# Kernel tuning notes

Hardware: AMD Instinct MI355X
Metric: run time of the kernel (lower is better)

## Reference

```python
import jax, jax.numpy as jnp
import numpy as np

N_NODES = 50000


def gcn_conv(x, src, dst, W, b, n_nodes):
    """PyG-style GCNConv: x' = D^-1/2 (A + I) D^-1/2 (x W) + b.
    src/dst already include self-loops."""
    h = x @ W  # [N, C_out]
    # symmetric normalization from degree (with self-loops, unit edge weight)
    deg = jax.ops.segment_sum(jnp.ones_like(dst, dtype=h.dtype), dst,
                              num_segments=n_nodes)  # [N]
    dinv = jnp.where(deg > 0, jax.lax.rsqrt(deg), 0.0)
    norm = dinv[src] * dinv[dst]  # [E]
    msg = h[src] * norm[:, None]  # gather + scale, [E, C_out]
    out = jax.ops.segment_sum(msg, dst, num_segments=n_nodes)  # scatter-add
    return out + b


def setup_inputs() -> dict:
    key = jax.random.key(0)
    k1, k2, k3, k4, k5, k6 = jax.random.split(key, 6)
    in_c, hid_c, out_c = 128, 64, 64
    x = jax.random.normal(k1, (N_NODES, in_c), dtype=jnp.float32)
    edge_index = jax.random.randint(k2, (2, 800000), 0, N_NODES, dtype=jnp.int64)
    # Glorot-ish init for weights, zeros for bias (as PyG default)
    W1 = jax.random.normal(k3, (in_c, hid_c), dtype=jnp.float32) / np.sqrt(in_c)
    b1 = jnp.zeros((hid_c,), dtype=jnp.float32)
    W2 = jax.random.normal(k4, (hid_c, out_c), dtype=jnp.float32) / np.sqrt(hid_c)
    b2 = jnp.zeros((out_c,), dtype=jnp.float32)
    return {"x": x, "edge_index": edge_index, "W1": W1, "b1": b1,
            "W2": W2, "b2": b2}


def reference(x, edge_index, W1, b1, W2, b2):
    n = x.shape[0]
    loops = jnp.arange(n, dtype=edge_index.dtype)
    src = jnp.concatenate([edge_index[0], loops])  # add self-loops
    dst = jnp.concatenate([edge_index[1], loops])
    h = gcn_conv(x, src, dst, W1, b1, n)
    h = jax.nn.relu(h)
    return gcn_conv(h, src, dst, W2, b2, n)
```

## Files before the change

### kernel.cpp

```cpp
#include <hip/hip_runtime.h>
#include <hip/hip_fp16.h>


#define C_HID 64

static inline size_t alignup(size_t x) { return (x + 255) & ~(size_t)255; }

typedef __attribute__((address_space(3))) unsigned int lds_uint;
typedef __attribute__((address_space(1))) const unsigned int glob_uint;

__device__ __forceinline__ int blockScanIncl256(int v, int* wsum) {
    const int lane = threadIdx.x & 63, wav = threadIdx.x >> 6;
    int s = v;
#pragma unroll
    for (int off = 1; off < 64; off <<= 1) {
        int t = __shfl_up(s, off);
        if (lane >= off) s += t;
    }
    if (lane == 63) wsum[wav] = s;
    __syncthreads();
    if (wav == 0 && lane < 4) {
        int ws = wsum[lane];
#pragma unroll
        for (int off = 1; off < 4; off <<= 1) {
            int t = __shfl_up(ws, off);
            if (lane >= off) ws += t;
        }
        wsum[lane] = ws;
    }
    __syncthreads();
    return (wav ? wsum[wav - 1] : 0) + s;
}

template <int K>
__global__ __launch_bounds__(256) void gemm1_hist_kernel(
    const float* __restrict__ X, const float* __restrict__ W,
    const int* __restrict__ dst, __half* __restrict__ outh,
    int* __restrict__ S, int n, int E, int ePer, int nb) {
    constexpr int KP = K + 4;
    __shared__ float Xs[64 * KP];
    __shared__ float Ws[K * 64];
    __shared__ int h[256];
    const int t = threadIdx.x;
    const int lane = t & 63;
    const int wav = t >> 6;

    if ((int)blockIdx.x < nb) {
        h[t] = 0;
        __syncthreads();
        int beg = blockIdx.x * ePer, end = min(E, beg + ePer);
        for (int e = beg + t; e < end; e += 256)
            atomicAdd(&h[dst[e] >> 8], 1);
        __syncthreads();
        for (int b = t; b < nb; b += 256)
            S[(size_t)b * nb + blockIdx.x] = h[b];
        return;
    }

    const int row0 = ((int)blockIdx.x - nb) * 64;
    {
        const char* gb = (const char*)W;
        char* lb = (char*)Ws;
        for (int off = wav * 1024; off < K * 64 * 4; off += 4096)
            __builtin_amdgcn_global_load_lds((glob_uint*)(gb + off + lane * 16),
                                             (lds_uint*)(lb + off), 16, 0, 0);
    }
    if (row0 + 64 <= n) {
        const float4* g4 = (const float4*)(X + (size_t)row0 * K);
        for (int i = t; i < 64 * (K / 4); i += 256) {
            float4 v = g4[i];
            int r = i / (K / 4), k0 = (i % (K / 4)) * 4;
            *(float4*)&Xs[r * KP + k0] = v;
        }
    } else {
        for (int i = t; i < 64 * K; i += 256) {
            int r = i / K, k = i % K;
            Xs[r * KP + k] = (row0 + r < n) ? X[(size_t)(row0 + r) * K + k] : 0.0f;
        }
    }
    __syncthreads();

    const int tx = t & 15;
    const int ty = t >> 4;
    float acc[4][4] = {{0.f}};
#pragma unroll 2
    for (int k0 = 0; k0 < K; k0 += 4) {
        float4 a0 = *(const float4*)&Xs[(4 * ty + 0) * KP + k0];
        float4 a1 = *(const float4*)&Xs[(4 * ty + 1) * KP + k0];
        float4 a2 = *(const float4*)&Xs[(4 * ty + 2) * KP + k0];
        float4 a3 = *(const float4*)&Xs[(4 * ty + 3) * KP + k0];
        float4 b0 = *(const float4*)&Ws[(k0 + 0) * 64 + 4 * tx];
        float4 b1 = *(const float4*)&Ws[(k0 + 1) * 64 + 4 * tx];
        float4 b2 = *(const float4*)&Ws[(k0 + 2) * 64 + 4 * tx];
        float4 b3 = *(const float4*)&Ws[(k0 + 3) * 64 + 4 * tx];
        const float* ap[4] = {(const float*)&a0, (const float*)&a1,
                              (const float*)&a2, (const float*)&a3};
        const float* bp[4] = {(const float*)&b0, (const float*)&b1,
                              (const float*)&b2, (const float*)&b3};
#pragma unroll
        for (int r = 0; r < 4; ++r)
#pragma unroll
            for (int kk = 0; kk < 4; ++kk) {
                float av = ap[r][kk];
#pragma unroll
                for (int c = 0; c < 4; ++c)
                    acc[r][c] = fmaf(av, bp[kk][c], acc[r][c]);
            }
    }
#pragma unroll
    for (int r = 0; r < 4; ++r) {
        int row = row0 + 4 * ty + r;
        if (row < n) {
            __half2 p01 = __floats2half2_rn(acc[r][0], acc[r][1]);
            __half2 p23 = __floats2half2_rn(acc[r][2], acc[r][3]);
            float2 st;
            ((__half2*)&st)[0] = p01;
            ((__half2*)&st)[1] = p23;
            *(float2*)&outh[(size_t)row * 64 + 4 * tx] = st;
        }
    }
}

__global__ __launch_bounds__(256) void scan_rows_kernel(
    int* __restrict__ S, int* __restrict__ T, int nb) {
    __shared__ int wsum[4];
    const int b = blockIdx.x, t = threadIdx.x;
    int v = (t < nb) ? S[(size_t)b * nb + t] : 0;
    int incl = blockScanIncl256(v, wsum);
    if (t < nb) S[(size_t)b * nb + t] = incl - v;
    if (t == 0) T[b] = wsum[3];
}

__global__ __launch_bounds__(256) void scatter_kernel(
    const int* __restrict__ src, const int* __restrict__ dst, int E, int ePer,
    const int* __restrict__ S, const int* __restrict__ T,
    unsigned* __restrict__ ebuf, int nb) {
    __shared__ int arr[256];
    __shared__ int wsum[4];
    const int b = blockIdx.x, t = threadIdx.x;
    int tv = (t < nb) ? T[t] : 0;
    int tincl = blockScanIncl256(tv, wsum);
    int texcl = tincl - tv;
    if (t < nb) arr[t] = S[(size_t)t * nb + b] + texcl;
    __syncthreads();
    int beg = b * ePer, end = min(E, beg + ePer);
    for (int e = beg + t; e < end; e += 256) {
        int d = dst[e];
        int s = src[e];
        int pos = atomicAdd(&arr[d >> 8], 1);
        ebuf[pos] = ((unsigned)s << 8) | (unsigned)(d & 255);
    }
}

__global__ __launch_bounds__(256) void build_kernel(
    const unsigned* __restrict__ ebuf, const int* __restrict__ T,
    int* __restrict__ row_ptr, float* __restrict__ dinv,
    int* __restrict__ esrc, int n, int nb) {
    __shared__ int arr[256];
    __shared__ int texcl_s[256];
    __shared__ int wsum[4];
    const int b = blockIdx.x, t = threadIdx.x;
    const int node0 = b << 8;

    int tv = (t < nb) ? T[t] : 0;
    int tincl = blockScanIncl256(tv, wsum);
    texcl_s[t] = tincl - tv;
    __syncthreads();
    const int ebeg = texcl_s[b];
    const int eend = (b + 1 < nb) ? texcl_s[b + 1] : wsum[3];

    arr[t] = 0;
    __syncthreads();
    for (int e = ebeg + t; e < eend; e += 256)
        atomicAdd(&arr[ebuf[e] & 255], 1);
    __syncthreads();
    int deg = arr[t];
    int incl = blockScanIncl256(deg, wsum);
    int excl = incl - deg;
    __syncthreads();
    arr[t] = ebeg + excl;
    int v = node0 + t;
    if (v < n) {
        row_ptr[v + 1] = ebeg + incl;
        dinv[v] = rsqrtf(1.0f + (float)deg);
        if (v == 0) row_ptr[0] = 0;
    }
    __syncthreads();
    for (int e = ebeg + t; e < eend; e += 256) {
        unsigned p = ebuf[e];
        int pos = atomicAdd(&arr[p & 255], 1);
        esrc[pos] = (int)(p >> 8);
    }
}

__global__ __launch_bounds__(256) void agg1_gemm2_kernel(
    const __half* __restrict__ g1, const int* __restrict__ row_ptr,
    const int* __restrict__ esrc, const float* __restrict__ dinv,
    const float* __restrict__ b1, const float* __restrict__ W2,
    __half* __restrict__ g2, int n) {
    __shared__ float Bt[64][68];
    __shared__ float Ws2[64 * 64];
    const int t = threadIdx.x, lane = t & 63, wav = t >> 6;

    {
        const char* gb = (const char*)W2;
        char* lb = (char*)Ws2;
        for (int off = wav * 1024; off < 64 * 64 * 4; off += 4096)
            __builtin_amdgcn_global_load_lds((glob_uint*)(gb + off + lane * 16),
                                             (lds_uint*)(lb + off), 16, 0, 0);
    }

    const int g = t >> 2;
    const int c = t & 3;
    const int row0 = blockIdx.x * 64;
    const int v = row0 + g;
    const float4* __restrict__ hs4 = (const float4*)g1;

    if (v < n) {
        float acc[16];
        float dv0 = dinv[v];
        {
            size_t rb = (size_t)v * 8 + 2 * c;
            float4 r0 = hs4[rb], r1 = hs4[rb + 1];
            const __half2* h0 = (const __half2*)&r0;
            const __half2* h1 = (const __half2*)&r1;
#pragma unroll
            for (int q = 0; q < 4; ++q) {
                float2 f0 = __half22float2(h0[q]);
                float2 f1 = __half22float2(h1[q]);
                acc[2 * q] = f0.x * dv0;     acc[2 * q + 1] = f0.y * dv0;
                acc[8 + 2 * q] = f1.x * dv0; acc[9 + 2 * q] = f1.y * dv0;
            }
        }
        const int beg = row_ptr[v], end = row_ptr[v + 1];
        int j = beg;
        for (; j + 4 <= end; j += 4) {
            int s0 = esrc[j], s1 = esrc[j + 1], s2 = esrc[j + 2], s3 = esrc[j + 3];
            float d0 = dinv[s0], d1 = dinv[s1], d2 = dinv[s2], d3 = dinv[s3];
            size_t rb0 = (size_t)s0 * 8 + 2 * c, rb1 = (size_t)s1 * 8 + 2 * c;
            size_t rb2 = (size_t)s2 * 8 + 2 * c, rb3 = (size_t)s3 * 8 + 2 * c;
            float4 a0 = hs4[rb0], a1 = hs4[rb0 + 1];
            float4 b0 = hs4[rb1], b1v = hs4[rb1 + 1];
            float4 c0 = hs4[rb2], c1 = hs4[rb2 + 1];
            float4 e0 = hs4[rb3], e1 = hs4[rb3 + 1];
            const __half2 *pa0 = (const __half2*)&a0, *pa1 = (const __half2*)&a1;
            const __half2 *pb0 = (const __half2*)&b0, *pb1 = (const __half2*)&b1v;
            const __half2 *pc0 = (const __half2*)&c0, *pc1 = (const __half2*)&c1;
            const __half2 *pe0 = (const __half2*)&e0, *pe1 = (const __half2*)&e1;
#pragma unroll
            for (int q = 0; q < 4; ++q) {
                float2 f;
                f = __half22float2(pa0[q]);
                acc[2 * q] = fmaf(f.x, d0, acc[2 * q]);
                acc[2 * q + 1] = fmaf(f.y, d0, acc[2 * q + 1]);
                f = __half22float2(pa1[q]);
                acc[8 + 2 * q] = fmaf(f.x, d0, acc[8 + 2 * q]);
                acc[9 + 2 * q] = fmaf(f.y, d0, acc[9 + 2 * q]);
                f = __half22float2(pb0[q]);
                acc[2 * q] = fmaf(f.x, d1, acc[2 * q]);
                acc[2 * q + 1] = fmaf(f.y, d1, acc[2 * q + 1]);
                f = __half22float2(pb1[q]);
                acc[8 + 2 * q] = fmaf(f.x, d1, acc[8 + 2 * q]);
                acc[9 + 2 * q] = fmaf(f.y, d1, acc[9 + 2 * q]);
                f = __half22float2(pc0[q]);
                acc[2 * q] = fmaf(f.x, d2, acc[2 * q]);
                acc[2 * q + 1] = fmaf(f.y, d2, acc[2 * q + 1]);
                f = __half22float2(pc1[q]);
                acc[8 + 2 * q] = fmaf(f.x, d2, acc[8 + 2 * q]);
                acc[9 + 2 * q] = fmaf(f.y, d2, acc[9 + 2 * q]);
                f = __half22float2(pe0[q]);
                acc[2 * q] = fmaf(f.x, d3, acc[2 * q]);
                acc[2 * q + 1] = fmaf(f.y, d3, acc[2 * q + 1]);
                f = __half22float2(pe1[q]);
                acc[8 + 2 * q] = fmaf(f.x, d3, acc[8 + 2 * q]);
                acc[9 + 2 * q] = fmaf(f.y, d3, acc[9 + 2 * q]);
            }
        }
        for (; j < end; ++j) {
            int s0 = esrc[j];
            float d0 = dinv[s0];
            size_t rb0 = (size_t)s0 * 8 + 2 * c;
            float4 a0 = hs4[rb0], a1 = hs4[rb0 + 1];
            const __half2 *pa0 = (const __half2*)&a0, *pa1 = (const __half2*)&a1;
#pragma unroll
            for (int q = 0; q < 4; ++q) {
                float2 f;
                f = __half22float2(pa0[q]);
                acc[2 * q] = fmaf(f.x, d0, acc[2 * q]);
                acc[2 * q + 1] = fmaf(f.y, d0, acc[2 * q + 1]);
                f = __half22float2(pa1[q]);
                acc[8 + 2 * q] = fmaf(f.x, d0, acc[8 + 2 * q]);
                acc[9 + 2 * q] = fmaf(f.y, d0, acc[9 + 2 * q]);
            }
        }
        const float* bb = b1 + c * 16;
#pragma unroll
        for (int u = 0; u < 4; ++u) {
            float4 w;
            w.x = fmaxf(fmaf(acc[4 * u + 0], dv0, bb[4 * u + 0]), 0.f);
            w.y = fmaxf(fmaf(acc[4 * u + 1], dv0, bb[4 * u + 1]), 0.f);
            w.z = fmaxf(fmaf(acc[4 * u + 2], dv0, bb[4 * u + 2]), 0.f);
            w.w = fmaxf(fmaf(acc[4 * u + 3], dv0, bb[4 * u + 3]), 0.f);
            *(float4*)&Bt[g][c * 16 + 4 * u] = w;
        }
    } else {
#pragma unroll
        for (int u = 0; u < 4; ++u)
            *(float4*)&Bt[g][c * 16 + 4 * u] = make_float4(0.f, 0.f, 0.f, 0.f);
    }
    __syncthreads();

    const int tx = t & 15;
    const int ty = t >> 4;
    float a2[4][4] = {{0.f}};
#pragma unroll 2
    for (int k0 = 0; k0 < 64; k0 += 4) {
        float4 x0 = *(const float4*)&Bt[4 * ty + 0][k0];
        float4 x1 = *(const float4*)&Bt[4 * ty + 1][k0];
        float4 x2 = *(const float4*)&Bt[4 * ty + 2][k0];
        float4 x3 = *(const float4*)&Bt[4 * ty + 3][k0];
        float4 w0 = *(const float4*)&Ws2[(k0 + 0) * 64 + 4 * tx];
        float4 w1 = *(const float4*)&Ws2[(k0 + 1) * 64 + 4 * tx];
        float4 w2 = *(const float4*)&Ws2[(k0 + 2) * 64 + 4 * tx];
        float4 w3 = *(const float4*)&Ws2[(k0 + 3) * 64 + 4 * tx];
        const float* xp[4] = {(const float*)&x0, (const float*)&x1,
                              (const float*)&x2, (const float*)&x3};
        const float* wp[4] = {(const float*)&w0, (const float*)&w1,
                              (const float*)&w2, (const float*)&w3};
#pragma unroll
        for (int r = 0; r < 4; ++r)
#pragma unroll
            for (int kk = 0; kk < 4; ++kk) {
                float av = xp[r][kk];
#pragma unroll
                for (int cc = 0; cc < 4; ++cc)
                    a2[r][cc] = fmaf(av, wp[kk][cc], a2[r][cc]);
            }
    }
#pragma unroll
    for (int r = 0; r < 4; ++r) {
        int row = row0 + 4 * ty + r;
        if (row < n) {
            float dv = dinv[row];
            __half2 p01 = __floats2half2_rn(a2[r][0] * dv, a2[r][1] * dv);
            __half2 p23 = __floats2half2_rn(a2[r][2] * dv, a2[r][3] * dv);
            float2 st;
            ((__half2*)&st)[0] = p01;
            ((__half2*)&st)[1] = p23;
            *(float2*)&g2[(size_t)row * 64 + 4 * tx] = st;
        }
    }
}

__global__ __launch_bounds__(256) void aggregate2_kernel(
    const __half* __restrict__ hs,
    const int* __restrict__ row_ptr,
    const int* __restrict__ esrc,
    const float* __restrict__ dinv,
    const float* __restrict__ bias,
    float* __restrict__ out, int n) {
    const int v = blockIdx.x * 32 + (threadIdx.x >> 3);
    if (v >= n) return;
    const int c8 = threadIdx.x & 7;
    const float4* __restrict__ hs4 = (const float4*)hs;

    const int beg = row_ptr[v];
    const int end = row_ptr[v + 1];

    float acc[8];
    {
        float4 raw = hs4[(size_t)v * 8 + c8];
        const __half2* hp = (const __half2*)&raw;
#pragma unroll
        for (int q = 0; q < 4; ++q) {
            float2 f = __half22float2(hp[q]);
            acc[2 * q] = f.x; acc[2 * q + 1] = f.y;
        }
    }

    int j = beg;
    for (; j + 4 <= end; j += 4) {
        int s0 = esrc[j], s1 = esrc[j + 1], s2 = esrc[j + 2], s3 = esrc[j + 3];
        float4 r0 = hs4[(size_t)s0 * 8 + c8];
        float4 r1 = hs4[(size_t)s1 * 8 + c8];
        float4 r2 = hs4[(size_t)s2 * 8 + c8];
        float4 r3 = hs4[(size_t)s3 * 8 + c8];
        const __half2* h0 = (const __half2*)&r0;
        const __half2* h1 = (const __half2*)&r1;
        const __half2* h2 = (const __half2*)&r2;
        const __half2* h3 = (const __half2*)&r3;
#pragma unroll
        for (int q = 0; q < 4; ++q) {
            float2 f0 = __half22float2(h0[q]);
            float2 f1 = __half22float2(h1[q]);
            float2 f2 = __half22float2(h2[q]);
            float2 f3 = __half22float2(h3[q]);
            acc[2 * q]     += (f0.x + f1.x) + (f2.x + f3.x);
            acc[2 * q + 1] += (f0.y + f1.y) + (f2.y + f3.y);
        }
    }
    for (; j < end; ++j) {
        int s0 = esrc[j];
        float4 r0 = hs4[(size_t)s0 * 8 + c8];
        const __half2* h0 = (const __half2*)&r0;
#pragma unroll
        for (int q = 0; q < 4; ++q) {
            float2 f0 = __half22float2(h0[q]);
            acc[2 * q] += f0.x;
            acc[2 * q + 1] += f0.y;
        }
    }

    float dv = dinv[v];
    float4 b0 = *(const float4*)(bias + c8 * 8);
    float4 b1v = *(const float4*)(bias + c8 * 8 + 4);
    float4 o0, o1;
    o0.x = fmaf(acc[0], dv, b0.x); o0.y = fmaf(acc[1], dv, b0.y);
    o0.z = fmaf(acc[2], dv, b0.z); o0.w = fmaf(acc[3], dv, b0.w);
    o1.x = fmaf(acc[4], dv, b1v.x); o1.y = fmaf(acc[5], dv, b1v.y);
    o1.z = fmaf(acc[6], dv, b1v.z); o1.w = fmaf(acc[7], dv, b1v.w);
    float4* op = (float4*)(out + (size_t)v * 64 + c8 * 8);
    op[0] = o0;
    op[1] = o1;
}

extern "C" void kernel_launch(void* const* d_in, const int* in_sizes, int n_in,
                              void* d_out, int out_size, void* d_ws, size_t ws_size,
                              hipStream_t stream) {
    const float* x  = (const float*)d_in[0];
    const int*   ei = (const int*)d_in[1];
    const float* W1 = (const float*)d_in[2];
    const float* b1 = (const float*)d_in[3];
    const float* W2 = (const float*)d_in[4];
    const float* b2 = (const float*)d_in[5];
    float* out = (float*)d_out;

    const int C_IN = 128;
    const int n = in_sizes[0] / C_IN;
    const int E = in_sizes[1] / 2;
    const int* src = ei;
    const int* dst = ei + E;

    const int nb = (n + 255) >> 8;
    const int ngb = (n + 63) / 64;
    const int ePer = (E + nb - 1) / nb;

    char* w = (char*)d_ws;
    float*    dinv    = (float*)w;    w += alignup((size_t)n * sizeof(float));
    __half*   g1      = (__half*)w;   w += alignup((size_t)n * C_HID * sizeof(__half));
    __half*   g2      = (__half*)w;   w += alignup((size_t)n * C_HID * sizeof(__half));
    int*      row_ptr = (int*)w;      w += alignup((size_t)(n + 1) * sizeof(int));
    int*      S       = (int*)w;      w += alignup((size_t)nb * nb * sizeof(int));
    int*      T       = (int*)w;      w += alignup((size_t)(nb + 1) * sizeof(int));
    unsigned* ebuf    = (unsigned*)w; w += alignup((size_t)E * sizeof(unsigned));
    int*      esrc    = (int*)w;

    gemm1_hist_kernel<128><<<nb + ngb, 256, 0, stream>>>(
        x, W1, dst, g1, S, n, E, ePer, nb);

    scan_rows_kernel<<<nb, 256, 0, stream>>>(S, T, nb);
    scatter_kernel<<<nb, 256, 0, stream>>>(src, dst, E, ePer, S, T, ebuf, nb);
    build_kernel<<<nb, 256, 0, stream>>>(ebuf, T, row_ptr, dinv, esrc, n, nb);

    agg1_gemm2_kernel<<<ngb, 256, 0, stream>>>(
        g1, row_ptr, esrc, dinv, b1, W2, g2, n);

    aggregate2_kernel<<<(n + 31) / 32, 256, 0, stream>>>(
        g2, row_ptr, esrc, dinv, b2, out, n);
}
```

Baseline: 161.4 us.

## Refine CSR bucketing to 64-node bins, prescale g1 by dinv, stage edges in LDS

The counting-sort CSR build now uses 64-node buckets with a fixed 512 edge chunks instead of 256-node buckets tied to the bucket count. This gives more parallel blocks in the build kernel and smaller per-block histograms. The build kernel now pre-scales g1 rows by dinv, so the first aggregation no longer gathers dinv per edge. Both aggregation kernels stage their block's edge-source list in shared memory when it fits, with a fallback to global reads. The cost is larger shared arrays, extra scan work over up to 1024 buckets, and an extra read-modify-write pass over g1.

```diff
diff --git a/kernel.cpp b/kernel.cpp
--- a/kernel.cpp
+++ b/kernel.cpp
@@ -3,6 +3,9 @@
 
 
 #define C_HID 64
+#define NCHUNK 512
+#define ES3 1280
+#define ES4 768
 
 static inline size_t alignup(size_t x) { return (x + 255) & ~(size_t)255; }
 
@@ -40,24 +43,24 @@
     constexpr int KP = K + 4;
     __shared__ float Xs[64 * KP];
     __shared__ float Ws[K * 64];
-    __shared__ int h[256];
+    __shared__ int h[1024];
     const int t = threadIdx.x;
     const int lane = t & 63;
     const int wav = t >> 6;
 
-    if ((int)blockIdx.x < nb) {
-        h[t] = 0;
+    if ((int)blockIdx.x < NCHUNK) {
+        for (int i = t; i < nb; i += 256) h[i] = 0;
         __syncthreads();
         int beg = blockIdx.x * ePer, end = min(E, beg + ePer);
         for (int e = beg + t; e < end; e += 256)
-            atomicAdd(&h[dst[e] >> 8], 1);
+            atomicAdd(&h[dst[e] >> 6], 1);
         __syncthreads();
         for (int b = t; b < nb; b += 256)
-            S[(size_t)b * nb + blockIdx.x] = h[b];
+            S[(size_t)b * NCHUNK + blockIdx.x] = h[b];
         return;
     }
 
-    const int row0 = ((int)blockIdx.x - nb) * 64;
+    const int row0 = ((int)blockIdx.x - NCHUNK) * 64;
     {
         const char* gb = (const char*)W;
         char* lb = (char*)Ws;
@@ -122,12 +125,19 @@
 }
 
 __global__ __launch_bounds__(256) void scan_rows_kernel(
-    int* __restrict__ S, int* __restrict__ T, int nb) {
+    int* __restrict__ S, int* __restrict__ T) {
     __shared__ int wsum[4];
     const int b = blockIdx.x, t = threadIdx.x;
-    int v = (t < nb) ? S[(size_t)b * nb + t] : 0;
-    int incl = blockScanIncl256(v, wsum);
-    if (t < nb) S[(size_t)b * nb + t] = incl - v;
+    int4 v = make_int4(0, 0, 0, 0);
+    if (t < NCHUNK / 4) v = ((const int4*)(S + (size_t)b * NCHUNK))[t];
+    int p1 = v.x + v.y, p2 = p1 + v.z, p3 = p2 + v.w;
+    int incl = blockScanIncl256(p3, wsum);
+    int excl = incl - p3;
+    if (t < NCHUNK / 4) {
+        int4 o;
+        o.x = excl; o.y = excl + v.x; o.z = excl + p1; o.w = excl + p2;
+        ((int4*)(S + (size_t)b * NCHUNK))[t] = o;
+    }
     if (t == 0) T[b] = wsum[3];
 }
 
@@ -135,61 +145,160 @@
     const int* __restrict__ src, const int* __restrict__ dst, int E, int ePer,
     const int* __restrict__ S, const int* __restrict__ T,
     unsigned* __restrict__ ebuf, int nb) {
-    __shared__ int arr[256];
+    __shared__ int tmp[1024];
+    __shared__ int arr[1024];
     __shared__ int wsum[4];
     const int b = blockIdx.x, t = threadIdx.x;
-    int tv = (t < nb) ? T[t] : 0;
-    int tincl = blockScanIncl256(tv, wsum);
-    int texcl = tincl - tv;
-    if (t < nb) arr[t] = S[(size_t)t * nb + b] + texcl;
+    {
+        int a0 = (4 * t + 0 < nb) ? T[4 * t + 0] : 0;
+        int a1 = (4 * t + 1 < nb) ? T[4 * t + 1] : 0;
+        int a2 = (4 * t + 2 < nb) ? T[4 * t + 2] : 0;
+        int a3 = (4 * t + 3 < nb) ? T[4 * t + 3] : 0;
+        int p1 = a0 + a1, p2 = p1 + a2, p3 = p2 + a3;
+        int incl = blockScanIncl256(p3, wsum);
+        int excl = incl - p3;
+        tmp[4 * t + 0] = excl;
+        tmp[4 * t + 1] = excl + a0;
+        tmp[4 * t + 2] = excl + p1;
+        tmp[4 * t + 3] = excl + p2;
+    }
+    __syncthreads();
+    for (int i = t; i < nb; i += 256)
+        arr[i] = S[(size_t)i * NCHUNK + b] + tmp[i];
     __syncthreads();
     int beg = b * ePer, end = min(E, beg + ePer);
     for (int e = beg + t; e < end; e += 256) {
         int d = dst[e];
         int s = src[e];
-        int pos = atomicAdd(&arr[d >> 8], 1);
-        ebuf[pos] = ((unsigned)s << 8) | (unsigned)(d & 255);
+        int pos = atomicAdd(&arr[d >> 6], 1);
+        ebuf[pos] = ((unsigned)s << 6) | (unsigned)(d & 63);
     }
 }
 
 __global__ __launch_bounds__(256) void build_kernel(
     const unsigned* __restrict__ ebuf, const int* __restrict__ T,
     int* __restrict__ row_ptr, float* __restrict__ dinv,
-    int* __restrict__ esrc, int n, int nb) {
-    __shared__ int arr[256];
-    __shared__ int texcl_s[256];
+    int* __restrict__ esrc, __half* __restrict__ g1, int n, int nb) {
+    __shared__ int tmp[1024];
+    __shared__ int cnt[64];
+    __shared__ int cur[64];
+    __shared__ float dvs[64];
     __shared__ int wsum[4];
     const int b = blockIdx.x, t = threadIdx.x;
-    const int node0 = b << 8;
-
-    int tv = (t < nb) ? T[t] : 0;
-    int tincl = blockScanIncl256(tv, wsum);
-    texcl_s[t] = tincl - tv;
-    __syncthreads();
-    const int ebeg = texcl_s[b];
-    const int eend = (b + 1 < nb) ? texcl_s[b + 1] : wsum[3];
-
-    arr[t] = 0;
-    __syncthreads();
+    {
+        int a0 = (4 * t + 0 < nb) ? T[4 * t + 0] : 0;
+        int a1 = (4 * t + 1 < nb) ? T[4 * t + 1] : 0;
+        int a2 = (4 * t + 2 < nb) ? T[4 * t + 2] : 0;
+        int a3 = (4 * t + 3 < nb) ? T[4 * t + 3] : 0;
+        int p1 = a0 + a1, p2 = p1 + a2, p3 = p2 + a3;
+        int incl = blockScanIncl256(p3, wsum);
+        int excl = incl - p3;
+        tmp[4 * t + 0] = excl + a0;
+        tmp[4 * t + 1] = excl + p1;
+        tmp[4 * t + 2] = excl + p2;
+        tmp[4 * t + 3] = excl + p3;
+    }
+    if (t < 64) cnt[t] = 0;
+    __syncthreads();
+    const int ebeg = b ? tmp[b - 1] : 0;
+    const int eend = tmp[b];
+
     for (int e = ebeg + t; e < eend; e += 256)
-        atomicAdd(&arr[ebuf[e] & 255], 1);
-    __syncthreads();
-    int deg = arr[t];
-    int incl = blockScanIncl256(deg, wsum);
-    int excl = incl - deg;
-    __syncthreads();
-    arr[t] = ebeg + excl;
-    int v = node0 + t;
-    if (v < n) {
-        row_ptr[v + 1] = ebeg + incl;
-        dinv[v] = rsqrtf(1.0f + (float)deg);
-        if (v == 0) row_ptr[0] = 0;
+        atomicAdd(&cnt[ebuf[e] & 63], 1);
+    __syncthreads();
+    if (t < 64) {
+        int deg = cnt[t];
+        int s = deg;
+#pragma unroll
+        for (int off = 1; off < 64; off <<= 1) {
+            int x = __shfl_up(s, off);
+            if (t >= off) s += x;
+        }
+        cur[t] = ebeg + s - deg;
+        float dv = rsqrtf(1.0f + (float)deg);
+        dvs[t] = dv;
+        int v = (b << 6) + t;
+        if (v < n) {
+            row_ptr[v + 1] = ebeg + s;
+            dinv[v] = dv;
+            if (v == 0) row_ptr[0] = 0;
+        }
     }
     __syncthreads();
     for (int e = ebeg + t; e < eend; e += 256) {
         unsigned p = ebuf[e];
-        int pos = atomicAdd(&arr[p & 255], 1);
-        esrc[pos] = (int)(p >> 8);
+        int pos = atomicAdd(&cur[p & 63], 1);
+        esrc[pos] = (int)(p >> 6);
+    }
+    {
+        const int row = t >> 2, q = t & 3;
+        const int v = (b << 6) + row;
+        if (v < n) {
+            float dv = dvs[row];
+            float4* gp = (float4*)(g1 + (size_t)v * 64 + q * 16);
+            float4 r0 = gp[0], r1 = gp[1];
+            __half2* h0 = (__half2*)&r0;
+            __half2* h1 = (__half2*)&r1;
+#pragma unroll
+            for (int i2 = 0; i2 < 4; ++i2) {
+                float2 f0 = __half22float2(h0[i2]);
+                float2 f1 = __half22float2(h1[i2]);
+                h0[i2] = __floats2half2_rn(f0.x * dv, f0.y * dv);
+                h1[i2] = __floats2half2_rn(f1.x * dv, f1.y * dv);
+            }
+            gp[0] = r0;
+            gp[1] = r1;
+        }
+    }
+}
+
+template <bool LDSE>
+__device__ __forceinline__ void agg1_body(
+    const float4* __restrict__ hs4, const int* es, const int* __restrict__ esg,
+    int beg0, int beg, int end, int c, float acc[16]) {
+    int j = beg;
+    for (; j + 4 <= end; j += 4) {
+        int s0, s1, s2, s3;
+        if (LDSE) {
+            s0 = es[j]; s1 = es[j + 1]; s2 = es[j + 2]; s3 = es[j + 3];
+        } else {
+            s0 = esg[beg0 + j]; s1 = esg[beg0 + j + 1];
+            s2 = esg[beg0 + j + 2]; s3 = esg[beg0 + j + 3];
+        }
+        size_t rb0 = (size_t)s0 * 8 + 2 * c, rb1 = (size_t)s1 * 8 + 2 * c;
+        size_t rb2 = (size_t)s2 * 8 + 2 * c, rb3 = (size_t)s3 * 8 + 2 * c;
+        float4 a0 = hs4[rb0], a1 = hs4[rb0 + 1];
+        float4 b0 = hs4[rb1], b1v = hs4[rb1 + 1];
+        float4 c0 = hs4[rb2], c1 = hs4[rb2 + 1];
+        float4 e0 = hs4[rb3], e1 = hs4[rb3 + 1];
+        const __half2 *pa0 = (const __half2*)&a0, *pa1 = (const __half2*)&a1;
+        const __half2 *pb0 = (const __half2*)&b0, *pb1 = (const __half2*)&b1v;
+        const __half2 *pc0 = (const __half2*)&c0, *pc1 = (const __half2*)&c1;
+        const __half2 *pe0 = (const __half2*)&e0, *pe1 = (const __half2*)&e1;
+#pragma unroll
+        for (int q = 0; q < 4; ++q) {
+            float2 f;
+            f = __half22float2(pa0[q]); acc[2 * q] += f.x; acc[2 * q + 1] += f.y;
+            f = __half22float2(pa1[q]); acc[8 + 2 * q] += f.x; acc[9 + 2 * q] += f.y;
+            f = __half22float2(pb0[q]); acc[2 * q] += f.x; acc[2 * q + 1] += f.y;
+            f = __half22float2(pb1[q]); acc[8 + 2 * q] += f.x; acc[9 + 2 * q] += f.y;
+            f = __half22float2(pc0[q]); acc[2 * q] += f.x; acc[2 * q + 1] += f.y;
+            f = __half22float2(pc1[q]); acc[8 + 2 * q] += f.x; acc[9 + 2 * q] += f.y;
+            f = __half22float2(pe0[q]); acc[2 * q] += f.x; acc[2 * q + 1] += f.y;
+            f = __half22float2(pe1[q]); acc[8 + 2 * q] += f.x; acc[9 + 2 * q] += f.y;
+        }
+    }
+    for (; j < end; ++j) {
+        int s0 = LDSE ? es[j] : esg[beg0 + j];
+        size_t rb0 = (size_t)s0 * 8 + 2 * c;
+        float4 a0 = hs4[rb0], a1 = hs4[rb0 + 1];
+        const __half2 *pa0 = (const __half2*)&a0, *pa1 = (const __half2*)&a1;
+#pragma unroll
+        for (int q = 0; q < 4; ++q) {
+            float2 f;
+            f = __half22float2(pa0[q]); acc[2 * q] += f.x; acc[2 * q + 1] += f.y;
+            f = __half22float2(pa1[q]); acc[8 + 2 * q] += f.x; acc[9 + 2 * q] += f.y;
+        }
     }
 }
 
@@ -200,7 +309,17 @@
     __half* __restrict__ g2, int n) {
     __shared__ float Bt[64][68];
     __shared__ float Ws2[64 * 64];
+    __shared__ int es[ES3];
     const int t = threadIdx.x, lane = t & 63, wav = t >> 6;
+    const int row0 = blockIdx.x * 64;
+
+    const int beg0 = row_ptr[row0];
+    const int end0 = row_ptr[min(row0 + 64, n)];
+    const int tot = end0 - beg0;
+    const bool uselds = (tot <= ES3);
+    if (uselds)
+        for (int i = t; i < tot; i += 256) es[i] = esrc[beg0 + i];
+    __syncthreads();
 
     {
         const char* gb = (const char*)W2;
@@ -212,13 +331,11 @@
 
     const int g = t >> 2;
     const int c = t & 3;
-    const int row0 = blockIdx.x * 64;
     const int v = row0 + g;
     const float4* __restrict__ hs4 = (const float4*)g1;
 
     if (v < n) {
         float acc[16];
-        float dv0 = dinv[v];
         {
             size_t rb = (size_t)v * 8 + 2 * c;
             float4 r0 = hs4[rb], r1 = hs4[rb + 1];
@@ -228,71 +345,15 @@
             for (int q = 0; q < 4; ++q) {
                 float2 f0 = __half22float2(h0[q]);
                 float2 f1 = __half22float2(h1[q]);
-                acc[2 * q] = f0.x * dv0;     acc[2 * q + 1] = f0.y * dv0;
-                acc[8 + 2 * q] = f1.x * dv0; acc[9 + 2 * q] = f1.y * dv0;
+                acc[2 * q] = f0.x;     acc[2 * q + 1] = f0.y;
+                acc[8 + 2 * q] = f1.x; acc[9 + 2 * q] = f1.y;
             }
         }
-        const int beg = row_ptr[v], end = row_ptr[v + 1];
-        int j = beg;
-        for (; j + 4 <= end; j += 4) {
-            int s0 = esrc[j], s1 = esrc[j + 1], s2 = esrc[j + 2], s3 = esrc[j + 3];
-            float d0 = dinv[s0], d1 = dinv[s1], d2 = dinv[s2], d3 = dinv[s3];
-            size_t rb0 = (size_t)s0 * 8 + 2 * c, rb1 = (size_t)s1 * 8 + 2 * c;
-            size_t rb2 = (size_t)s2 * 8 + 2 * c, rb3 = (size_t)s3 * 8 + 2 * c;
-            float4 a0 = hs4[rb0], a1 = hs4[rb0 + 1];
-            float4 b0 = hs4[rb1], b1v = hs4[rb1 + 1];
-            float4 c0 = hs4[rb2], c1 = hs4[rb2 + 1];
-            float4 e0 = hs4[rb3], e1 = hs4[rb3 + 1];
-            const __half2 *pa0 = (const __half2*)&a0, *pa1 = (const __half2*)&a1;
-            const __half2 *pb0 = (const __half2*)&b0, *pb1 = (const __half2*)&b1v;
-            const __half2 *pc0 = (const __half2*)&c0, *pc1 = (const __half2*)&c1;
-            const __half2 *pe0 = (const __half2*)&e0, *pe1 = (const __half2*)&e1;
-#pragma unroll
-            for (int q = 0; q < 4; ++q) {
-                float2 f;
-                f = __half22float2(pa0[q]);
-                acc[2 * q] = fmaf(f.x, d0, acc[2 * q]);
-                acc[2 * q + 1] = fmaf(f.y, d0, acc[2 * q + 1]);
-                f = __half22float2(pa1[q]);
-                acc[8 + 2 * q] = fmaf(f.x, d0, acc[8 + 2 * q]);
-                acc[9 + 2 * q] = fmaf(f.y, d0, acc[9 + 2 * q]);
-                f = __half22float2(pb0[q]);
-                acc[2 * q] = fmaf(f.x, d1, acc[2 * q]);
-                acc[2 * q + 1] = fmaf(f.y, d1, acc[2 * q + 1]);
-                f = __half22float2(pb1[q]);
-                acc[8 + 2 * q] = fmaf(f.x, d1, acc[8 + 2 * q]);
-                acc[9 + 2 * q] = fmaf(f.y, d1, acc[9 + 2 * q]);
-                f = __half22float2(pc0[q]);
-                acc[2 * q] = fmaf(f.x, d2, acc[2 * q]);
-                acc[2 * q + 1] = fmaf(f.y, d2, acc[2 * q + 1]);
-                f = __half22float2(pc1[q]);
-                acc[8 + 2 * q] = fmaf(f.x, d2, acc[8 + 2 * q]);
-                acc[9 + 2 * q] = fmaf(f.y, d2, acc[9 + 2 * q]);
-                f = __half22float2(pe0[q]);
-                acc[2 * q] = fmaf(f.x, d3, acc[2 * q]);
-                acc[2 * q + 1] = fmaf(f.y, d3, acc[2 * q + 1]);
-                f = __half22float2(pe1[q]);
-                acc[8 + 2 * q] = fmaf(f.x, d3, acc[8 + 2 * q]);
-                acc[9 + 2 * q] = fmaf(f.y, d3, acc[9 + 2 * q]);
-            }
-        }
-        for (; j < end; ++j) {
-            int s0 = esrc[j];
-            float d0 = dinv[s0];
-            size_t rb0 = (size_t)s0 * 8 + 2 * c;
-            float4 a0 = hs4[rb0], a1 = hs4[rb0 + 1];
-            const __half2 *pa0 = (const __half2*)&a0, *pa1 = (const __half2*)&a1;
-#pragma unroll
-            for (int q = 0; q < 4; ++q) {
-                float2 f;
-                f = __half22float2(pa0[q]);
-                acc[2 * q] = fmaf(f.x, d0, acc[2 * q]);
-                acc[2 * q + 1] = fmaf(f.y, d0, acc[2 * q + 1]);
-                f = __half22float2(pa1[q]);
-                acc[8 + 2 * q] = fmaf(f.x, d0, acc[8 + 2 * q]);
-                acc[9 + 2 * q] = fmaf(f.y, d0, acc[9 + 2 * q]);
-            }
-        }
+        const int beg = row_ptr[v] - beg0;
+        const int end = row_ptr[v + 1] - beg0;
+        if (uselds) agg1_body<true>(hs4, es, esrc, beg0, beg, end, c, acc);
+        else        agg1_body<false>(hs4, es, esrc, beg0, beg, end, c, acc);
+        const float dv0 = dinv[v];
         const float* bb = b1 + c * 16;
 #pragma unroll
         for (int u = 0; u < 4; ++u) {
@@ -352,35 +413,19 @@
     }
 }
 
-__global__ __launch_bounds__(256) void aggregate2_kernel(
-    const __half* __restrict__ hs,
-    const int* __restrict__ row_ptr,
-    const int* __restrict__ esrc,
-    const float* __restrict__ dinv,
-    const float* __restrict__ bias,
-    float* __restrict__ out, int n) {
-    const int v = blockIdx.x * 32 + (threadIdx.x >> 3);
-    if (v >= n) return;
-    const int c8 = threadIdx.x & 7;
-    const float4* __restrict__ hs4 = (const float4*)hs;
-
-    const int beg = row_ptr[v];
-    const int end = row_ptr[v + 1];
-
-    float acc[8];
-    {
-        float4 raw = hs4[(size_t)v * 8 + c8];
-        const __half2* hp = (const __half2*)&raw;
-#pragma unroll
-        for (int q = 0; q < 4; ++q) {
-            float2 f = __half22float2(hp[q]);
-            acc[2 * q] = f.x; acc[2 * q + 1] = f.y;
-        }
-    }
-
+template <bool LDSE>
+__device__ __forceinline__ void agg2_body(
+    const float4* __restrict__ hs4, const int* es, const int* __restrict__ esg,
+    int beg0, int beg, int end, int c8, float acc[8]) {
     int j = beg;
     for (; j + 4 <= end; j += 4) {
-        int s0 = esrc[j], s1 = esrc[j + 1], s2 = esrc[j + 2], s3 = esrc[j + 3];
+        int s0, s1, s2, s3;
+        if (LDSE) {
+            s0 = es[j]; s1 = es[j + 1]; s2 = es[j + 2]; s3 = es[j + 3];
+        } else {
+            s0 = esg[beg0 + j]; s1 = esg[beg0 + j + 1];
+            s2 = esg[beg0 + j + 2]; s3 = esg[beg0 + j + 3];
+        }
         float4 r0 = hs4[(size_t)s0 * 8 + c8];
         float4 r1 = hs4[(size_t)s1 * 8 + c8];
         float4 r2 = hs4[(size_t)s2 * 8 + c8];
@@ -400,7 +445,7 @@
         }
     }
     for (; j < end; ++j) {
-        int s0 = esrc[j];
+        int s0 = LDSE ? es[j] : esg[beg0 + j];
         float4 r0 = hs4[(size_t)s0 * 8 + c8];
         const __half2* h0 = (const __half2*)&r0;
 #pragma unroll
@@ -410,6 +455,46 @@
             acc[2 * q + 1] += f0.y;
         }
     }
+}
+
+__global__ __launch_bounds__(256) void aggregate2_kernel(
+    const __half* __restrict__ hs,
+    const int* __restrict__ row_ptr,
+    const int* __restrict__ esrc,
+    const float* __restrict__ dinv,
+    const float* __restrict__ bias,
+    float* __restrict__ out, int n) {
+    __shared__ int es[ES4];
+    const int t = threadIdx.x;
+    const int row0 = blockIdx.x * 32;
+    const int beg0 = row_ptr[row0];
+    const int end0 = row_ptr[min(row0 + 32, n)];
+    const int tot = end0 - beg0;
+    const bool uselds = (tot <= ES4);
+    if (uselds)
+        for (int i = t; i < tot; i += 256) es[i] = esrc[beg0 + i];
+    __syncthreads();
+
+    const int v = row0 + (t >> 3);
+    if (v >= n) return;
+    const int c8 = t & 7;
+    const float4* __restrict__ hs4 = (const float4*)hs;
+
+    float acc[8];
+    {
+        float4 raw = hs4[(size_t)v * 8 + c8];
+        const __half2* hp = (const __half2*)&raw;
+#pragma unroll
+        for (int q = 0; q < 4; ++q) {
+            float2 f = __half22float2(hp[q]);
+            acc[2 * q] = f.x; acc[2 * q + 1] = f.y;
+        }
+    }
+
+    const int beg = row_ptr[v] - beg0;
+    const int end = row_ptr[v + 1] - beg0;
+    if (uselds) agg2_body<true>(hs4, es, esrc, beg0, beg, end, c8, acc);
+    else        agg2_body<false>(hs4, es, esrc, beg0, beg, end, c8, acc);
 
     float dv = dinv[v];
     float4 b0 = *(const float4*)(bias + c8 * 8);
@@ -441,26 +526,26 @@
     const int* src = ei;
     const int* dst = ei + E;
 
-    const int nb = (n + 255) >> 8;
+    const int nb = (n + 63) >> 6;
     const int ngb = (n + 63) / 64;
-    const int ePer = (E + nb - 1) / nb;
+    const int ePer = (E + NCHUNK - 1) / NCHUNK;
 
     char* w = (char*)d_ws;
     float*    dinv    = (float*)w;    w += alignup((size_t)n * sizeof(float));
     __half*   g1      = (__half*)w;   w += alignup((size_t)n * C_HID * sizeof(__half));
     __half*   g2      = (__half*)w;   w += alignup((size_t)n * C_HID * sizeof(__half));
     int*      row_ptr = (int*)w;      w += alignup((size_t)(n + 1) * sizeof(int));
-    int*      S       = (int*)w;      w += alignup((size_t)nb * nb * sizeof(int));
+    int*      S       = (int*)w;      w += alignup((size_t)nb * NCHUNK * sizeof(int));
     int*      T       = (int*)w;      w += alignup((size_t)(nb + 1) * sizeof(int));
     unsigned* ebuf    = (unsigned*)w; w += alignup((size_t)E * sizeof(unsigned));
     int*      esrc    = (int*)w;
 
-    gemm1_hist_kernel<128><<<nb + ngb, 256, 0, stream>>>(
+    gemm1_hist_kernel<128><<<NCHUNK + ngb, 256, 0, stream>>>(
         x, W1, dst, g1, S, n, E, ePer, nb);
 
-    scan_rows_kernel<<<nb, 256, 0, stream>>>(S, T, nb);
-    scatter_kernel<<<nb, 256, 0, stream>>>(src, dst, E, ePer, S, T, ebuf, nb);
-    build_kernel<<<nb, 256, 0, stream>>>(ebuf, T, row_ptr, dinv, esrc, n, nb);
+    scan_rows_kernel<<<nb, 256, 0, stream>>>(S, T);
+    scatter_kernel<<<NCHUNK, 256, 0, stream>>>(src, dst, E, ePer, S, T, ebuf, nb);
+    build_kernel<<<nb, 256, 0, stream>>>(ebuf, T, row_ptr, dinv, esrc, g1, n, nb);
 
     agg1_gemm2_kernel<<<ngb, 256, 0, stream>>>(
         g1, row_ptr, esrc, dinv, b1, W2, g2, n);
```

Measured after the change: 163.9 us. Within noise of the previous version (+1.5%).
